# Performance work log

Hardware: AMD Instinct MI355X
Metric: run time of the kernel (lower is better)

The kernel has to match this reference:

```python
import jax, jax.numpy as jnp
import numpy as np

L = 16
IN0 = 7  # 3 + 3 + 1 per the torch module
CH = [16, 32, 16]
N = 500000
NEG_SLOPE = 0.2


def setup_inputs() -> dict:
    key = jax.random.key(0)
    ks = jax.random.split(key, 5)
    x = jax.random.normal(ks[0], (N, IN0), dtype=jnp.float32)
    idx = jax.random.randint(ks[1], (N,), 0, L, dtype=jnp.int32)
    # kaiming-uniform-like init scale per layer fan-in
    def init_w(k, shape):
        fan_in = shape[1]
        bound = float(np.sqrt(6.0 / fan_in))
        return jax.random.uniform(k, shape, dtype=jnp.float32, minval=-bound, maxval=bound)
    W0 = init_w(ks[2], (L, IN0, CH[0]))
    W1 = init_w(ks[3], (L, CH[0], CH[1]))
    W2 = init_w(ks[4], (L, CH[1], CH[2]))
    b0 = jnp.zeros((L, CH[0]), dtype=jnp.float32)
    b1 = jnp.zeros((L, CH[1]), dtype=jnp.float32)
    b2 = jnp.zeros((L, CH[2]), dtype=jnp.float32)
    return {"x": x, "idx": idx, "W0": W0, "b0": b0, "W1": W1, "b1": b1, "W2": W2, "b2": b2}


def reference(x, idx, W0, b0, W1, b1, W2, b2):
    # Per-point expert-indexed MLP: h <- LeakyReLU(h @ W[idx] + b[idx]) per layer.
    h = x
    for W, b in ((W0, b0), (W1, b1), (W2, b2)):
        # gather per-point weight [N, in, out] and bias [N, out], vec-mat per point
        h = jax.nn.leaky_relu(
            jnp.einsum("nc,nco->no", h, W[idx]) + b[idx],
            negative_slope=NEG_SLOPE,
        )
    return h
```

## Files before the change

### kernel.cpp

```cpp
#include <hip/hip_runtime.h>
#include <hip/hip_fp16.h>


#define L_EXP 16
#define IN0   7
#define C0    16
#define C1    32
#define C2    16
#define NEG   0.2f
#define BLK   256
#define MPT   2

typedef _Float16 h2 __attribute__((ext_vector_type(2)));
union F4H { float4 f4; h2 h[4]; };

__device__ __forceinline__ h2 pk(float a, float b) {
    return __builtin_bit_cast(h2, __builtin_amdgcn_cvt_pkrtz(a, b));
}
__device__ __forceinline__ float leaky(float a) { return fmaxf(a, NEG * a); }
__device__ __forceinline__ float fdot2(h2 a, h2 b, float c) {
    return __builtin_amdgcn_fdot2(a, b, c, false);
}

__global__ void __launch_bounds__(BLK, 4) k_fused(
    const float* __restrict__ x, const int* __restrict__ idx,
    const float* __restrict__ W0, const float* __restrict__ b0,
    const float* __restrict__ W1, const float* __restrict__ b1,
    const float* __restrict__ W2, const float* __restrict__ b2,
    float* __restrict__ out, int n) {
    __shared__ __align__(16) __half sW0[C0 * L_EXP * 8];
    __shared__ __align__(16) __half sW1[C1 * 2 * L_EXP * 8];
    __shared__ __align__(16) __half sW2[C2 * 4 * L_EXP * 8];
    __shared__ float sB1[C1 * L_EXP];
    __shared__ float sB2[C2 * L_EXP];

    int t = threadIdx.x;

    {
        int o = t >> 4, e = t & 15;
        float v0 = W0[e * (IN0 * C0) + 0 * C0 + o];
        float v1 = W0[e * (IN0 * C0) + 1 * C0 + o];
        float v2 = W0[e * (IN0 * C0) + 2 * C0 + o];
        float v3 = W0[e * (IN0 * C0) + 3 * C0 + o];
        float v4 = W0[e * (IN0 * C0) + 4 * C0 + o];
        float v5 = W0[e * (IN0 * C0) + 5 * C0 + o];
        float v6 = W0[e * (IN0 * C0) + 6 * C0 + o];
        float v7 = b0[e * C0 + o];
        F4H u;
        u.h[0] = pk(v0, v1); u.h[1] = pk(v2, v3);
        u.h[2] = pk(v4, v5); u.h[3] = pk(v6, v7);
        reinterpret_cast<float4*>(sW0)[t] = u.f4;
    }
#pragma unroll
    for (int rr = 0; rr < 4; ++rr) {
        int r = rr * BLK + t;
        int o = r >> 5, q = (r >> 4) & 1, e = r & 15;
        const float* wp = W1 + e * (C0 * C1) + (q * 8) * C1 + o;
        F4H u;
#pragma unroll
        for (int j = 0; j < 4; ++j)
            u.h[j] = pk(wp[(2 * j) * C1], wp[(2 * j + 1) * C1]);
        reinterpret_cast<float4*>(sW1)[r] = u.f4;
    }
#pragma unroll
    for (int rr = 0; rr < 4; ++rr) {
        int r = rr * BLK + t;
        int o = r >> 6, q = (r >> 4) & 3, e = r & 15;
        const float* wp = W2 + e * (C1 * C2) + (q * 8) * C2 + o;
        F4H u;
#pragma unroll
        for (int j = 0; j < 4; ++j)
            u.h[j] = pk(wp[(2 * j) * C2], wp[(2 * j + 1) * C2]);
        reinterpret_cast<float4*>(sW2)[r] = u.f4;
    }
    {
        int o = t >> 4, e = t & 15;
        sB1[t] = b1[e * C1 + o];
        int r2 = t + 256; int o2 = r2 >> 4, e2 = r2 & 15;
        sB1[r2] = b1[e2 * C1 + o2];
        sB2[t] = b2[e * C2 + o];
    }
    __syncthreads();

    int base = blockIdx.x * (BLK * MPT);
#pragma unroll 1
    for (int m = 0; m < MPT; ++m) {
        int i = base + m * BLK + t;
        bool act = (i < n);
        int ii = act ? i : (n - 1);
        int e = idx[ii] & 15;

        const float* xp = x + (size_t)ii * IN0;
        float x0 = xp[0], x1 = xp[1], x2 = xp[2], x3 = xp[3];
        float x4 = xp[4], x5 = xp[5], x6 = xp[6];
        h2 xh0 = pk(x0, x1), xh1 = pk(x2, x3);
        h2 xh2 = pk(x4, x5), xh3 = pk(x6, 1.0f);

        const char* w0p = (const char*)sW0 + e * 16;
        const char* w1p = (const char*)sW1 + e * 16;
        const char* w2p = (const char*)sW2 + e * 16;

        h2 h0h[8];
#pragma unroll
        for (int op = 0; op < 8; ++op) {
            F4H ua, ub;
            ua.f4 = *reinterpret_cast<const float4*>(w0p + (2 * op) * 256);
            ub.f4 = *reinterpret_cast<const float4*>(w0p + (2 * op + 1) * 256);
            float a0 = 0.f, a1 = 0.f;
            a0 = fdot2(xh0, ua.h[0], a0); a1 = fdot2(xh0, ub.h[0], a1);
            a0 = fdot2(xh1, ua.h[1], a0); a1 = fdot2(xh1, ub.h[1], a1);
            a0 = fdot2(xh2, ua.h[2], a0); a1 = fdot2(xh2, ub.h[2], a1);
            a0 = fdot2(xh3, ua.h[3], a0); a1 = fdot2(xh3, ub.h[3], a1);
            h0h[op] = pk(leaky(a0), leaky(a1));
        }

        h2 tvh[16];
#pragma unroll
        for (int op = 0; op < 16; ++op) {
            F4H ua, ub, uc, ud;
            ua.f4 = *reinterpret_cast<const float4*>(w1p + (4 * op + 0) * 256);
            ub.f4 = *reinterpret_cast<const float4*>(w1p + (4 * op + 1) * 256);
            uc.f4 = *reinterpret_cast<const float4*>(w1p + (4 * op + 2) * 256);
            ud.f4 = *reinterpret_cast<const float4*>(w1p + (4 * op + 3) * 256);
            float a0 = sB1[(2 * op) * 16 + e];
            float a1 = sB1[(2 * op + 1) * 16 + e];
#pragma unroll
            for (int p = 0; p < 4; ++p) {
                a0 = fdot2(h0h[p], ua.h[p], a0);
                a1 = fdot2(h0h[p], uc.h[p], a1);
            }
#pragma unroll
            for (int p = 0; p < 4; ++p) {
                a0 = fdot2(h0h[4 + p], ub.h[p], a0);
                a1 = fdot2(h0h[4 + p], ud.h[p], a1);
            }
            tvh[op] = pk(leaky(a0), leaky(a1));
        }

        float4 ov[4];
#pragma unroll
        for (int o = 0; o < C2; ++o) {
            F4H ua, ub, uc, ud;
            ua.f4 = *reinterpret_cast<const float4*>(w2p + (4 * o + 0) * 256);
            ub.f4 = *reinterpret_cast<const float4*>(w2p + (4 * o + 1) * 256);
            uc.f4 = *reinterpret_cast<const float4*>(w2p + (4 * o + 2) * 256);
            ud.f4 = *reinterpret_cast<const float4*>(w2p + (4 * o + 3) * 256);
            float a = sB2[o * 16 + e];
#pragma unroll
            for (int p = 0; p < 4; ++p) a = fdot2(tvh[p],      ua.h[p], a);
#pragma unroll
            for (int p = 0; p < 4; ++p) a = fdot2(tvh[4 + p],  ub.h[p], a);
#pragma unroll
            for (int p = 0; p < 4; ++p) a = fdot2(tvh[8 + p],  uc.h[p], a);
#pragma unroll
            for (int p = 0; p < 4; ++p) a = fdot2(tvh[12 + p], ud.h[p], a);
            float r = leaky(a);
            if ((o & 3) == 0) ov[o >> 2].x = r;
            else if ((o & 3) == 1) ov[o >> 2].y = r;
            else if ((o & 3) == 2) ov[o >> 2].z = r;
            else ov[o >> 2].w = r;
        }

        if (act) {
            float4* op = reinterpret_cast<float4*>(out + (size_t)i * C2);
            op[0] = ov[0]; op[1] = ov[1]; op[2] = ov[2]; op[3] = ov[3];
        }
    }
}

extern "C" void kernel_launch(void* const* d_in, const int* in_sizes, int n_in,
                              void* d_out, int out_size, void* d_ws, size_t ws_size,
                              hipStream_t stream) {
    const float* x  = (const float*)d_in[0];
    const int*  idx = (const int*)d_in[1];
    const float* W0 = (const float*)d_in[2];
    const float* b0 = (const float*)d_in[3];
    const float* W1 = (const float*)d_in[4];
    const float* b1 = (const float*)d_in[5];
    const float* W2 = (const float*)d_in[6];
    const float* b2 = (const float*)d_in[7];
    float* out = (float*)d_out;

    int n = in_sizes[1];
    int blocks = (n + BLK * MPT - 1) / (BLK * MPT);
    k_fused<<<blocks, BLK, 0, stream>>>(x, idx, W0, b0, W1, b1, W2, b2, out, n);
}
```

Measured before the change: 127.8 us.

## Sort points by expert within each block and interleave two points per thread

Each block bins its 512 points by expert index using shared-memory atomics and a shuffle prefix scan, then gives each thread two sorted points. Neighbouring lanes therefore mostly share an expert, which is meant to cut LDS bank conflicts and divergence in the per-expert weight reads. Processing two independent points per thread interleaves their dot-product chains to raise ILP. The cost is extra barriers, atomics, scattered x loads and output stores, and higher register pressure. The x row is now read with two overlapping unaligned float4 loads, which over-reads past the end of the last row, and the b2 bias is stored in half precision.

```diff
diff --git a/kernel.cpp b/kernel.cpp
--- a/kernel.cpp
+++ b/kernel.cpp
@@ -9,7 +9,7 @@
 #define C2    16
 #define NEG   0.2f
 #define BLK   256
-#define MPT   2
+#define PPB   512
 
 typedef _Float16 h2 __attribute__((ext_vector_type(2)));
 union F4H { float4 f4; h2 h[4]; };
@@ -31,8 +31,11 @@
     __shared__ __align__(16) __half sW0[C0 * L_EXP * 8];
     __shared__ __align__(16) __half sW1[C1 * 2 * L_EXP * 8];
     __shared__ __align__(16) __half sW2[C2 * 4 * L_EXP * 8];
-    __shared__ float sB1[C1 * L_EXP];
-    __shared__ float sB2[C2 * L_EXP];
+    __shared__ float  sB1[C1 * L_EXP];
+    __shared__ __half sB2h[C2 * L_EXP];
+    __shared__ unsigned short spid[PPB];
+    __shared__ int bins[L_EXP];
+    __shared__ int poff[L_EXP];
 
     int t = threadIdx.x;
 
@@ -78,93 +81,156 @@
         sB1[t] = b1[e * C1 + o];
         int r2 = t + 256; int o2 = r2 >> 4, e2 = r2 & 15;
         sB1[r2] = b1[e2 * C1 + o2];
-        sB2[t] = b2[e * C2 + o];
-    }
-    __syncthreads();
-
-    int base = blockIdx.x * (BLK * MPT);
-#pragma unroll 1
-    for (int m = 0; m < MPT; ++m) {
-        int i = base + m * BLK + t;
-        bool act = (i < n);
-        int ii = act ? i : (n - 1);
-        int e = idx[ii] & 15;
-
-        const float* xp = x + (size_t)ii * IN0;
-        float x0 = xp[0], x1 = xp[1], x2 = xp[2], x3 = xp[3];
-        float x4 = xp[4], x5 = xp[5], x6 = xp[6];
-        h2 xh0 = pk(x0, x1), xh1 = pk(x2, x3);
-        h2 xh2 = pk(x4, x5), xh3 = pk(x6, 1.0f);
-
-        const char* w0p = (const char*)sW0 + e * 16;
-        const char* w1p = (const char*)sW1 + e * 16;
-        const char* w2p = (const char*)sW2 + e * 16;
-
-        h2 h0h[8];
-#pragma unroll
-        for (int op = 0; op < 8; ++op) {
-            F4H ua, ub;
-            ua.f4 = *reinterpret_cast<const float4*>(w0p + (2 * op) * 256);
-            ub.f4 = *reinterpret_cast<const float4*>(w0p + (2 * op + 1) * 256);
-            float a0 = 0.f, a1 = 0.f;
-            a0 = fdot2(xh0, ua.h[0], a0); a1 = fdot2(xh0, ub.h[0], a1);
-            a0 = fdot2(xh1, ua.h[1], a0); a1 = fdot2(xh1, ub.h[1], a1);
-            a0 = fdot2(xh2, ua.h[2], a0); a1 = fdot2(xh2, ub.h[2], a1);
-            a0 = fdot2(xh3, ua.h[3], a0); a1 = fdot2(xh3, ub.h[3], a1);
-            h0h[op] = pk(leaky(a0), leaky(a1));
-        }
-
-        h2 tvh[16];
-#pragma unroll
-        for (int op = 0; op < 16; ++op) {
-            F4H ua, ub, uc, ud;
-            ua.f4 = *reinterpret_cast<const float4*>(w1p + (4 * op + 0) * 256);
-            ub.f4 = *reinterpret_cast<const float4*>(w1p + (4 * op + 1) * 256);
-            uc.f4 = *reinterpret_cast<const float4*>(w1p + (4 * op + 2) * 256);
-            ud.f4 = *reinterpret_cast<const float4*>(w1p + (4 * op + 3) * 256);
-            float a0 = sB1[(2 * op) * 16 + e];
-            float a1 = sB1[(2 * op + 1) * 16 + e];
-#pragma unroll
-            for (int p = 0; p < 4; ++p) {
-                a0 = fdot2(h0h[p], ua.h[p], a0);
-                a1 = fdot2(h0h[p], uc.h[p], a1);
-            }
-#pragma unroll
-            for (int p = 0; p < 4; ++p) {
-                a0 = fdot2(h0h[4 + p], ub.h[p], a0);
-                a1 = fdot2(h0h[4 + p], ud.h[p], a1);
-            }
-            tvh[op] = pk(leaky(a0), leaky(a1));
-        }
-
-        float4 ov[4];
-#pragma unroll
-        for (int o = 0; o < C2; ++o) {
-            F4H ua, ub, uc, ud;
-            ua.f4 = *reinterpret_cast<const float4*>(w2p + (4 * o + 0) * 256);
-            ub.f4 = *reinterpret_cast<const float4*>(w2p + (4 * o + 1) * 256);
-            uc.f4 = *reinterpret_cast<const float4*>(w2p + (4 * o + 2) * 256);
-            ud.f4 = *reinterpret_cast<const float4*>(w2p + (4 * o + 3) * 256);
-            float a = sB2[o * 16 + e];
-#pragma unroll
-            for (int p = 0; p < 4; ++p) a = fdot2(tvh[p],      ua.h[p], a);
-#pragma unroll
-            for (int p = 0; p < 4; ++p) a = fdot2(tvh[4 + p],  ub.h[p], a);
-#pragma unroll
-            for (int p = 0; p < 4; ++p) a = fdot2(tvh[8 + p],  uc.h[p], a);
-#pragma unroll
-            for (int p = 0; p < 4; ++p) a = fdot2(tvh[12 + p], ud.h[p], a);
-            float r = leaky(a);
-            if ((o & 3) == 0) ov[o >> 2].x = r;
-            else if ((o & 3) == 1) ov[o >> 2].y = r;
-            else if ((o & 3) == 2) ov[o >> 2].z = r;
-            else ov[o >> 2].w = r;
-        }
-
-        if (act) {
-            float4* op = reinterpret_cast<float4*>(out + (size_t)i * C2);
-            op[0] = ov[0]; op[1] = ov[1]; op[2] = ov[2]; op[3] = ov[3];
-        }
+        sB2h[t] = __float2half(b2[e * C2 + o]);
+    }
+    if (t < L_EXP) bins[t] = 0;
+    __syncthreads();
+
+    int base = blockIdx.x * PPB;
+    int cnt = n - base; if (cnt > PPB) cnt = PPB;
+    int e0 = 0, r0 = 0, e1 = 0, r1 = 0;
+    bool v0 = (t < cnt), v1 = (t + 256 < cnt);
+    if (v0) { e0 = idx[base + t] & 15;       r0 = atomicAdd(&bins[e0], 1); }
+    if (v1) { e1 = idx[base + t + 256] & 15; r1 = atomicAdd(&bins[e1], 1); }
+    __syncthreads();
+    if (t < L_EXP) {
+        int c = bins[t], s = c;
+#pragma unroll
+        for (int d = 1; d < L_EXP; d <<= 1) {
+            int u = __shfl_up(s, d, L_EXP);
+            if (t >= d) s += u;
+        }
+        poff[t] = s - c;
+    }
+    __syncthreads();
+    if (v0) spid[poff[e0] + r0] = (unsigned short)((e0 << 9) | t);
+    if (v1) spid[poff[e1] + r1] = (unsigned short)((e1 << 9) | (t + 256));
+    __syncthreads();
+
+    bool act0 = (t < cnt), act1 = (t + 256 < cnt);
+    int sp0 = act0 ? (int)spid[t] : 0;
+    int sp1 = act1 ? (int)spid[t + 256] : 0;
+    int eP = sp0 >> 9, pidP = base + (sp0 & 511);
+    int eQ = sp1 >> 9, pidQ = base + (sp1 & 511);
+
+    const float* xpP = x + (size_t)pidP * IN0;
+    const float* xpQ = x + (size_t)pidQ * IN0;
+    float4 aP = *reinterpret_cast<const float4*>(xpP);
+    float4 bP = *reinterpret_cast<const float4*>(xpP + 3);
+    float4 aQ = *reinterpret_cast<const float4*>(xpQ);
+    float4 bQ = *reinterpret_cast<const float4*>(xpQ + 3);
+    h2 xP0 = pk(aP.x, aP.y), xP1 = pk(aP.z, aP.w);
+    h2 xP2 = pk(bP.y, bP.z), xP3 = pk(bP.w, 1.0f);
+    h2 xQ0 = pk(aQ.x, aQ.y), xQ1 = pk(aQ.z, aQ.w);
+    h2 xQ2 = pk(bQ.y, bQ.z), xQ3 = pk(bQ.w, 1.0f);
+
+    const char* w0P = (const char*)sW0 + eP * 16;
+    const char* w1P = (const char*)sW1 + eP * 16;
+    const char* w2P = (const char*)sW2 + eP * 16;
+    const char* w0Q = (const char*)sW0 + eQ * 16;
+    const char* w1Q = (const char*)sW1 + eQ * 16;
+    const char* w2Q = (const char*)sW2 + eQ * 16;
+
+    h2 hP[8], hQ[8];
+#pragma unroll
+    for (int op = 0; op < 8; ++op) {
+        F4H uaP, ubP, uaQ, ubQ;
+        uaP.f4 = *reinterpret_cast<const float4*>(w0P + (2 * op) * 256);
+        ubP.f4 = *reinterpret_cast<const float4*>(w0P + (2 * op + 1) * 256);
+        uaQ.f4 = *reinterpret_cast<const float4*>(w0Q + (2 * op) * 256);
+        ubQ.f4 = *reinterpret_cast<const float4*>(w0Q + (2 * op + 1) * 256);
+        float p0 = 0.f, p1 = 0.f, q0 = 0.f, q1 = 0.f;
+        p0 = fdot2(xP0, uaP.h[0], p0); p1 = fdot2(xP0, ubP.h[0], p1);
+        q0 = fdot2(xQ0, uaQ.h[0], q0); q1 = fdot2(xQ0, ubQ.h[0], q1);
+        p0 = fdot2(xP1, uaP.h[1], p0); p1 = fdot2(xP1, ubP.h[1], p1);
+        q0 = fdot2(xQ1, uaQ.h[1], q0); q1 = fdot2(xQ1, ubQ.h[1], q1);
+        p0 = fdot2(xP2, uaP.h[2], p0); p1 = fdot2(xP2, ubP.h[2], p1);
+        q0 = fdot2(xQ2, uaQ.h[2], q0); q1 = fdot2(xQ2, ubQ.h[2], q1);
+        p0 = fdot2(xP3, uaP.h[3], p0); p1 = fdot2(xP3, ubP.h[3], p1);
+        q0 = fdot2(xQ3, uaQ.h[3], q0); q1 = fdot2(xQ3, ubQ.h[3], q1);
+        hP[op] = pk(leaky(p0), leaky(p1));
+        hQ[op] = pk(leaky(q0), leaky(q1));
+    }
+    __builtin_amdgcn_sched_barrier(0);
+
+    h2 tP[16], tQ[16];
+#pragma unroll
+    for (int op = 0; op < 16; ++op) {
+        F4H uaP, ubP, ucP, udP, uaQ, ubQ, ucQ, udQ;
+        uaP.f4 = *reinterpret_cast<const float4*>(w1P + (4 * op + 0) * 256);
+        ubP.f4 = *reinterpret_cast<const float4*>(w1P + (4 * op + 1) * 256);
+        ucP.f4 = *reinterpret_cast<const float4*>(w1P + (4 * op + 2) * 256);
+        udP.f4 = *reinterpret_cast<const float4*>(w1P + (4 * op + 3) * 256);
+        uaQ.f4 = *reinterpret_cast<const float4*>(w1Q + (4 * op + 0) * 256);
+        ubQ.f4 = *reinterpret_cast<const float4*>(w1Q + (4 * op + 1) * 256);
+        ucQ.f4 = *reinterpret_cast<const float4*>(w1Q + (4 * op + 2) * 256);
+        udQ.f4 = *reinterpret_cast<const float4*>(w1Q + (4 * op + 3) * 256);
+        float p0 = sB1[(2 * op) * 16 + eP];
+        float p1 = sB1[(2 * op + 1) * 16 + eP];
+        float q0 = sB1[(2 * op) * 16 + eQ];
+        float q1 = sB1[(2 * op + 1) * 16 + eQ];
+#pragma unroll
+        for (int p = 0; p < 4; ++p) {
+            p0 = fdot2(hP[p], uaP.h[p], p0);
+            p1 = fdot2(hP[p], ucP.h[p], p1);
+            q0 = fdot2(hQ[p], uaQ.h[p], q0);
+            q1 = fdot2(hQ[p], ucQ.h[p], q1);
+        }
+#pragma unroll
+        for (int p = 0; p < 4; ++p) {
+            p0 = fdot2(hP[4 + p], ubP.h[p], p0);
+            p1 = fdot2(hP[4 + p], udP.h[p], p1);
+            q0 = fdot2(hQ[4 + p], ubQ.h[p], q0);
+            q1 = fdot2(hQ[4 + p], udQ.h[p], q1);
+        }
+        tP[op] = pk(leaky(p0), leaky(p1));
+        tQ[op] = pk(leaky(q0), leaky(q1));
+    }
+    __builtin_amdgcn_sched_barrier(0);
+
+    float4* outP = reinterpret_cast<float4*>(out + (size_t)pidP * C2);
+    float4* outQ = reinterpret_cast<float4*>(out + (size_t)pidQ * C2);
+#pragma unroll
+    for (int og = 0; og < 4; ++og) {
+        float4 oP, oQ;
+#pragma unroll
+        for (int j = 0; j < 4; ++j) {
+            int o = og * 4 + j;
+            F4H uaP, ubP, ucP, udP, uaQ, ubQ, ucQ, udQ;
+            uaP.f4 = *reinterpret_cast<const float4*>(w2P + (4 * o + 0) * 256);
+            ubP.f4 = *reinterpret_cast<const float4*>(w2P + (4 * o + 1) * 256);
+            ucP.f4 = *reinterpret_cast<const float4*>(w2P + (4 * o + 2) * 256);
+            udP.f4 = *reinterpret_cast<const float4*>(w2P + (4 * o + 3) * 256);
+            uaQ.f4 = *reinterpret_cast<const float4*>(w2Q + (4 * o + 0) * 256);
+            ubQ.f4 = *reinterpret_cast<const float4*>(w2Q + (4 * o + 1) * 256);
+            ucQ.f4 = *reinterpret_cast<const float4*>(w2Q + (4 * o + 2) * 256);
+            udQ.f4 = *reinterpret_cast<const float4*>(w2Q + (4 * o + 3) * 256);
+            float ap = __half2float(sB2h[o * 16 + eP]);
+            float aq = __half2float(sB2h[o * 16 + eQ]);
+#pragma unroll
+            for (int p = 0; p < 4; ++p) ap = fdot2(tP[p],      uaP.h[p], ap);
+#pragma unroll
+            for (int p = 0; p < 4; ++p) ap = fdot2(tP[4 + p],  ubP.h[p], ap);
+#pragma unroll
+            for (int p = 0; p < 4; ++p) ap = fdot2(tP[8 + p],  ucP.h[p], ap);
+#pragma unroll
+            for (int p = 0; p < 4; ++p) ap = fdot2(tP[12 + p], udP.h[p], ap);
+#pragma unroll
+            for (int p = 0; p < 4; ++p) aq = fdot2(tQ[p],      uaQ.h[p], aq);
+#pragma unroll
+            for (int p = 0; p < 4; ++p) aq = fdot2(tQ[4 + p],  ubQ.h[p], aq);
+#pragma unroll
+            for (int p = 0; p < 4; ++p) aq = fdot2(tQ[8 + p],  ucQ.h[p], aq);
+#pragma unroll
+            for (int p = 0; p < 4; ++p) aq = fdot2(tQ[12 + p], udQ.h[p], aq);
+            float rp = leaky(ap), rq = leaky(aq);
+            if (j == 0) { oP.x = rp; oQ.x = rq; }
+            else if (j == 1) { oP.y = rp; oQ.y = rq; }
+            else if (j == 2) { oP.z = rp; oQ.z = rq; }
+            else { oP.w = rp; oQ.w = rq; }
+        }
+        if (act0) outP[og] = oP;
+        if (act1) outQ[og] = oQ;
     }
 }
 
@@ -182,6 +248,6 @@
     float* out = (float*)d_out;
 
     int n = in_sizes[1];
-    int blocks = (n + BLK * MPT - 1) / (BLK * MPT);
+    int blocks = (n + PPB - 1) / PPB;
     k_fused<<<blocks, BLK, 0, stream>>>(x, idx, W0, b0, W1, b1, W2, b2, out, n);
 }
```

After: 305.3 us. 139% more time.

## Bucket points by expert per block so each thread reuses weights across four points

Applied to the files above, without the earlier changes.

Each block now takes 976 points and counting-sorts them by expert in LDS, using atomics, a shuffle-based prefix sum and per-expert padding to multiples of four. Each thread then processes four points that share an expert, so every weight vector read from LDS feeds four dot products instead of one, cutting LDS bandwidth per point. Layers 2 and 3 are interleaved in chunks of 8 hidden units to bound register use. The layer-3 bias is now stored in half precision, and launch bounds drop to 2 blocks per SIMD. The cost is sort overhead, scattered per-point global loads and stores, and more register pressure with lower occupancy.

```diff
diff --git a/kernel.cpp b/kernel.cpp
--- a/kernel.cpp
+++ b/kernel.cpp
@@ -9,7 +9,7 @@
 #define C2    16
 #define NEG   0.2f
 #define BLK   256
-#define MPT   2
+#define PPB   976
 
 typedef _Float16 h2 __attribute__((ext_vector_type(2)));
 union F4H { float4 f4; h2 h[4]; };
@@ -22,7 +22,7 @@
     return __builtin_amdgcn_fdot2(a, b, c, false);
 }
 
-__global__ void __launch_bounds__(BLK, 4) k_fused(
+__global__ void __launch_bounds__(BLK, 2) k_fused(
     const float* __restrict__ x, const int* __restrict__ idx,
     const float* __restrict__ W0, const float* __restrict__ b0,
     const float* __restrict__ W1, const float* __restrict__ b1,
@@ -31,8 +31,11 @@
     __shared__ __align__(16) __half sW0[C0 * L_EXP * 8];
     __shared__ __align__(16) __half sW1[C1 * 2 * L_EXP * 8];
     __shared__ __align__(16) __half sW2[C2 * 4 * L_EXP * 8];
-    __shared__ float sB1[C1 * L_EXP];
-    __shared__ float sB2[C2 * L_EXP];
+    __shared__ float  sB1[C1 * L_EXP];
+    __shared__ __half sB2h[C2 * L_EXP];
+    __shared__ unsigned short spid[1024];
+    __shared__ int bins[L_EXP];
+    __shared__ int poff[L_EXP];
 
     int t = threadIdx.x;
 
@@ -78,92 +81,162 @@
         sB1[t] = b1[e * C1 + o];
         int r2 = t + 256; int o2 = r2 >> 4, e2 = r2 & 15;
         sB1[r2] = b1[e2 * C1 + o2];
-        sB2[t] = b2[e * C2 + o];
-    }
-    __syncthreads();
-
-    int base = blockIdx.x * (BLK * MPT);
+        sB2h[t] = __float2half(b2[e * C2 + o]);
+    }
+    if (t < L_EXP) bins[t] = 0;
+    {
+        reinterpret_cast<int*>(spid)[t] = -1;
+        reinterpret_cast<int*>(spid)[t + 256] = -1;
+    }
+    __syncthreads();
+
+    int base = blockIdx.x * PPB;
+    int cnt = n - base; if (cnt > PPB) cnt = PPB;
+    int eL[4], rL[4];
+    bool vL[4];
+    int i4 = t * 4;
+#pragma unroll
+    for (int q = 0; q < 4; ++q) {
+        int li = i4 + q;
+        vL[q] = (li < cnt);
+        if (vL[q]) {
+            eL[q] = idx[base + li] & 15;
+            rL[q] = atomicAdd(&bins[eL[q]], 1);
+        }
+    }
+    __syncthreads();
+    if (t < L_EXP) {
+        int c = bins[t];
+        int p = (c + 3) & ~3;
+        int s = p;
+#pragma unroll
+        for (int d = 1; d < L_EXP; d <<= 1) {
+            int u = __shfl_up(s, d, L_EXP);
+            if (t >= d) s += u;
+        }
+        poff[t] = s - p;
+    }
+    __syncthreads();
+#pragma unroll
+    for (int q = 0; q < 4; ++q)
+        if (vL[q]) spid[poff[eL[q]] + rL[q]] =
+            (unsigned short)((eL[q] << 10) | (i4 + q));
+    __syncthreads();
+
+    int s0 = (int)spid[4 * t];
+    bool any = (s0 != 0xFFFF);
+    int e = any ? (s0 >> 10) : 0;
+    int l0 = any ? (s0 & 1023) : 0;
+    int pid[4]; bool act[4];
+#pragma unroll
+    for (int q = 0; q < 4; ++q) {
+        int sq = (int)spid[4 * t + q];
+        act[q] = (sq != 0xFFFF);
+        pid[q] = base + (act[q] ? (sq & 1023) : l0);
+    }
+
+    const char* w0p = (const char*)sW0 + e * 16;
+    const char* w1p = (const char*)sW1 + e * 16;
+    const char* w2p = (const char*)sW2 + e * 16;
+
+    h2 xh[4][4];
+#pragma unroll
+    for (int q = 0; q < 4; ++q) {
+        const float* xp = x + (size_t)pid[q] * IN0;
+        float4 a = *reinterpret_cast<const float4*>(xp);
+        float4 b = *reinterpret_cast<const float4*>(xp + 3);
+        xh[q][0] = pk(a.x, a.y);
+        xh[q][1] = pk(a.z, a.w);
+        xh[q][2] = pk(b.y, b.z);
+        xh[q][3] = pk(b.w, 1.0f);
+    }
+    __builtin_amdgcn_sched_barrier(0);
+
+    h2 h0h[4][8];
+#pragma unroll
+    for (int op = 0; op < 8; ++op) {
+        F4H ua, ub;
+        ua.f4 = *reinterpret_cast<const float4*>(w0p + (2 * op) * 256);
+        ub.f4 = *reinterpret_cast<const float4*>(w0p + (2 * op + 1) * 256);
+#pragma unroll
+        for (int q = 0; q < 4; ++q) {
+            float a0 = 0.f, a1 = 0.f;
+            a0 = fdot2(xh[q][0], ua.h[0], a0); a1 = fdot2(xh[q][0], ub.h[0], a1);
+            a0 = fdot2(xh[q][1], ua.h[1], a0); a1 = fdot2(xh[q][1], ub.h[1], a1);
+            a0 = fdot2(xh[q][2], ua.h[2], a0); a1 = fdot2(xh[q][2], ub.h[2], a1);
+            a0 = fdot2(xh[q][3], ua.h[3], a0); a1 = fdot2(xh[q][3], ub.h[3], a1);
+            h0h[q][op] = pk(leaky(a0), leaky(a1));
+        }
+    }
+    __builtin_amdgcn_sched_barrier(0);
+
+    float h2a[4][C2];
+#pragma unroll
+    for (int q = 0; q < 4; ++q)
+#pragma unroll
+        for (int o = 0; o < C2; ++o)
+            h2a[q][o] = __half2float(sB2h[o * 16 + e]);
 #pragma unroll 1
-    for (int m = 0; m < MPT; ++m) {
-        int i = base + m * BLK + t;
-        bool act = (i < n);
-        int ii = act ? i : (n - 1);
-        int e = idx[ii] & 15;
-
-        const float* xp = x + (size_t)ii * IN0;
-        float x0 = xp[0], x1 = xp[1], x2 = xp[2], x3 = xp[3];
-        float x4 = xp[4], x5 = xp[5], x6 = xp[6];
-        h2 xh0 = pk(x0, x1), xh1 = pk(x2, x3);
-        h2 xh2 = pk(x4, x5), xh3 = pk(x6, 1.0f);
-
-        const char* w0p = (const char*)sW0 + e * 16;
-        const char* w1p = (const char*)sW1 + e * 16;
-        const char* w2p = (const char*)sW2 + e * 16;
-
-        h2 h0h[8];
-#pragma unroll
-        for (int op = 0; op < 8; ++op) {
+    for (int ch = 0; ch < 4; ++ch) {
+        float tvf[4][8];
+#pragma unroll
+        for (int o8 = 0; o8 < 8; ++o8) {
+            int o = ch * 8 + o8;
             F4H ua, ub;
-            ua.f4 = *reinterpret_cast<const float4*>(w0p + (2 * op) * 256);
-            ub.f4 = *reinterpret_cast<const float4*>(w0p + (2 * op + 1) * 256);
-            float a0 = 0.f, a1 = 0.f;
-            a0 = fdot2(xh0, ua.h[0], a0); a1 = fdot2(xh0, ub.h[0], a1);
-            a0 = fdot2(xh1, ua.h[1], a0); a1 = fdot2(xh1, ub.h[1], a1);
-            a0 = fdot2(xh2, ua.h[2], a0); a1 = fdot2(xh2, ub.h[2], a1);
-            a0 = fdot2(xh3, ua.h[3], a0); a1 = fdot2(xh3, ub.h[3], a1);
-            h0h[op] = pk(leaky(a0), leaky(a1));
-        }
-
-        h2 tvh[16];
-#pragma unroll
-        for (int op = 0; op < 16; ++op) {
-            F4H ua, ub, uc, ud;
-            ua.f4 = *reinterpret_cast<const float4*>(w1p + (4 * op + 0) * 256);
-            ub.f4 = *reinterpret_cast<const float4*>(w1p + (4 * op + 1) * 256);
-            uc.f4 = *reinterpret_cast<const float4*>(w1p + (4 * op + 2) * 256);
-            ud.f4 = *reinterpret_cast<const float4*>(w1p + (4 * op + 3) * 256);
-            float a0 = sB1[(2 * op) * 16 + e];
-            float a1 = sB1[(2 * op + 1) * 16 + e];
-#pragma unroll
-            for (int p = 0; p < 4; ++p) {
-                a0 = fdot2(h0h[p], ua.h[p], a0);
-                a1 = fdot2(h0h[p], uc.h[p], a1);
+            ua.f4 = *reinterpret_cast<const float4*>(w1p + (2 * o) * 256);
+            ub.f4 = *reinterpret_cast<const float4*>(w1p + (2 * o + 1) * 256);
+            float bias = sB1[o * 16 + e];
+#pragma unroll
+            for (int q = 0; q < 4; ++q) {
+                float a = bias;
+                a = fdot2(h0h[q][0], ua.h[0], a);
+                a = fdot2(h0h[q][1], ua.h[1], a);
+                a = fdot2(h0h[q][2], ua.h[2], a);
+                a = fdot2(h0h[q][3], ua.h[3], a);
+                a = fdot2(h0h[q][4], ub.h[0], a);
+                a = fdot2(h0h[q][5], ub.h[1], a);
+                a = fdot2(h0h[q][6], ub.h[2], a);
+                a = fdot2(h0h[q][7], ub.h[3], a);
+                tvf[q][o8] = leaky(a);
             }
-#pragma unroll
-            for (int p = 0; p < 4; ++p) {
-                a0 = fdot2(h0h[4 + p], ub.h[p], a0);
-                a1 = fdot2(h0h[4 + p], ud.h[p], a1);
+        }
+        __builtin_amdgcn_sched_barrier(0);
+        h2 tvh[4][4];
+#pragma unroll
+        for (int q = 0; q < 4; ++q)
+#pragma unroll
+            for (int p = 0; p < 4; ++p)
+                tvh[q][p] = pk(tvf[q][2 * p], tvf[q][2 * p + 1]);
+#pragma unroll
+        for (int o = 0; o < C2; ++o) {
+            F4H u;
+            u.f4 = *reinterpret_cast<const float4*>(w2p + (4 * o + ch) * 256);
+#pragma unroll
+            for (int q = 0; q < 4; ++q) {
+                float a = h2a[q][o];
+                a = fdot2(tvh[q][0], u.h[0], a);
+                a = fdot2(tvh[q][1], u.h[1], a);
+                a = fdot2(tvh[q][2], u.h[2], a);
+                a = fdot2(tvh[q][3], u.h[3], a);
+                h2a[q][o] = a;
             }
-            tvh[op] = pk(leaky(a0), leaky(a1));
-        }
-
-        float4 ov[4];
-#pragma unroll
-        for (int o = 0; o < C2; ++o) {
-            F4H ua, ub, uc, ud;
-            ua.f4 = *reinterpret_cast<const float4*>(w2p + (4 * o + 0) * 256);
-            ub.f4 = *reinterpret_cast<const float4*>(w2p + (4 * o + 1) * 256);
-            uc.f4 = *reinterpret_cast<const float4*>(w2p + (4 * o + 2) * 256);
-            ud.f4 = *reinterpret_cast<const float4*>(w2p + (4 * o + 3) * 256);
-            float a = sB2[o * 16 + e];
-#pragma unroll
-            for (int p = 0; p < 4; ++p) a = fdot2(tvh[p],      ua.h[p], a);
-#pragma unroll
-            for (int p = 0; p < 4; ++p) a = fdot2(tvh[4 + p],  ub.h[p], a);
-#pragma unroll
-            for (int p = 0; p < 4; ++p) a = fdot2(tvh[8 + p],  uc.h[p], a);
-#pragma unroll
-            for (int p = 0; p < 4; ++p) a = fdot2(tvh[12 + p], ud.h[p], a);
-            float r = leaky(a);
-            if ((o & 3) == 0) ov[o >> 2].x = r;
-            else if ((o & 3) == 1) ov[o >> 2].y = r;
-            else if ((o & 3) == 2) ov[o >> 2].z = r;
-            else ov[o >> 2].w = r;
-        }
-
-        if (act) {
-            float4* op = reinterpret_cast<float4*>(out + (size_t)i * C2);
-            op[0] = ov[0]; op[1] = ov[1]; op[2] = ov[2]; op[3] = ov[3];
+        }
+        __builtin_amdgcn_sched_barrier(0);
+    }
+
+#pragma unroll
+    for (int q = 0; q < 4; ++q) {
+        if (act[q]) {
+            float4* outp = reinterpret_cast<float4*>(out + (size_t)pid[q] * C2);
+#pragma unroll
+            for (int og = 0; og < 4; ++og) {
+                float4 o;
+                o.x = leaky(h2a[q][og * 4 + 0]);
+                o.y = leaky(h2a[q][og * 4 + 1]);
+                o.z = leaky(h2a[q][og * 4 + 2]);
+                o.w = leaky(h2a[q][og * 4 + 3]);
+                outp[og] = o;
+            }
         }
     }
 }
@@ -182,6 +255,6 @@
     float* out = (float*)d_out;
 
     int n = in_sizes[1];
-    int blocks = (n + BLK * MPT - 1) / (BLK * MPT);
+    int blocks = (n + PPB - 1) / PPB;
     k_fused<<<blocks, BLK, 0, stream>>>(x, idx, W0, b0, W1, b1, W2, b2, out, n);
 }
```

After: 123.0 us. -3.7%, faster.
